# Optimization experiments

Measured on AMD Instinct MI355X. Metric: run time of the kernel, lower is better.

Reference implementation:

```python
import jax, jax.numpy as jnp
import numpy as np

B, T, I, H = 512, 1024, 50, 32  # batch, seq_len, input_size, hidden_size


def setup_inputs() -> dict:
    key = jax.random.key(0)
    ks = jax.random.split(key, 13)
    s = 1.0 / np.sqrt(H)  # PyTorch LSTM/Linear uniform init bound

    def u(k, shape):
        return jax.random.uniform(k, shape, jnp.float32, -s, s)

    return {
        "x": jax.random.normal(ks[0], (B, T, I), jnp.float32),
        # forward direction LSTM params (gate order: i, f, g, o)
        "w_ih_f": u(ks[1], (4 * H, I)),
        "w_hh_f": u(ks[2], (4 * H, H)),
        "b_ih_f": u(ks[3], (4 * H,)),
        "b_hh_f": u(ks[4], (4 * H,)),
        # reverse direction LSTM params
        "w_ih_r": u(ks[5], (4 * H, I)),
        "w_hh_r": u(ks[6], (4 * H, H)),
        "b_ih_r": u(ks[7], (4 * H,)),
        "b_hh_r": u(ks[8], (4 * H,)),
        # FC head
        "fc1_w": u(ks[9], (2 * H, 2 * H)),
        "fc1_b": u(ks[10], (2 * H,)),
        "fc3_w": u(ks[11], (1, 2 * H)),
        "fc3_b": u(ks[12], (1,)),
    }


def _lstm_scan(x_proj, w_hh):
    # x_proj: (T, B, 4H) = precomputed input projections + biases
    b = x_proj.shape[1]
    h0 = jnp.zeros((b, H), x_proj.dtype)
    c0 = jnp.zeros((b, H), x_proj.dtype)

    def step(carry, xp):
        h, c = carry
        z = xp + h @ w_hh.T  # (B, 4H)
        i, f, g, o = jnp.split(z, 4, axis=-1)
        c = jax.nn.sigmoid(f) * c + jax.nn.sigmoid(i) * jnp.tanh(g)
        h = jax.nn.sigmoid(o) * jnp.tanh(c)
        return (h, c), h

    _, hs = jax.lax.scan(step, (h0, c0), x_proj)
    return hs  # (T, B, H)


def reference(x, w_ih_f, w_hh_f, b_ih_f, b_hh_f,
              w_ih_r, w_hh_r, b_ih_r, b_hh_r,
              fc1_w, fc1_b, fc3_w, fc3_b):
    xt = jnp.swapaxes(x, 0, 1)  # (T, B, I) time-major for scan
    # batch all input projections up front (big GEMM instead of per-step)
    pf = xt @ w_ih_f.T + (b_ih_f + b_hh_f)          # (T, B, 4H)
    pr = xt[::-1] @ w_ih_r.T + (b_ih_r + b_hh_r)    # reversed time

    hf = _lstm_scan(pf, w_hh_f)           # (T, B, H)
    hr = _lstm_scan(pr, w_hh_r)[::-1]     # flip back to forward time order

    out = jnp.concatenate([hf, hr], axis=-1)  # (T, B, 2H)
    out = jnp.swapaxes(out, 0, 1)             # (B, T, 2H)
    out = out @ fc1_w.T + fc1_b               # fc1
    # dropout(p=0.2) is identity in eval/inference mode
    out = out @ fc3_w.T + fc3_b               # fc3 -> (B, T, 1)
    return out
```

## Files before the change

kernel.cpp:

```cpp
#include <hip/hip_runtime.h>

#define BB 512
#define TT 1024
#define II 50
#define HH 32
#define CH 16
#define NCH (TT / CH)
#define RSLOT 32

typedef float v2f __attribute__((ext_vector_type(2)));
typedef float v4f __attribute__((ext_vector_type(4)));
typedef short v8s __attribute__((ext_vector_type(8)));

__device__ __forceinline__ float fast_rcp(float x) { return __builtin_amdgcn_rcpf(x); }
__device__ __forceinline__ float sigm(float x) { return fast_rcp(1.f + __expf(-x)); }
__device__ __forceinline__ float tanh_(float x) {
    return 1.f - 2.f * fast_rcp(1.f + __expf(2.f * x));
}
__device__ __forceinline__ short bf16rne(float f) {
    unsigned u = __float_as_uint(f);
    u += 0x7FFF + ((u >> 16) & 1);
    return (short)(u >> 16);
}
__device__ __forceinline__ float rlane(float v, int l) {
    return __int_as_float(__builtin_amdgcn_readlane(__float_as_int(v), l));
}

#if __has_builtin(__builtin_amdgcn_permlane32_swap)
typedef unsigned v2u __attribute__((ext_vector_type(2)));
__device__ __forceinline__ float xhalf_sum(float p) {
    v2u r = __builtin_amdgcn_permlane32_swap(__float_as_uint(p),
                                             __float_as_uint(p), false, false);
    return __uint_as_float(r.x) + __uint_as_float(r.y);
}
#else
__device__ __forceinline__ float xhalf_sum(float p) {
    return p + __shfl_xor(p, 32, 64);
}
#endif

__global__ void init_out_kernel(float* __restrict__ out,
                                const float* __restrict__ fc1_b,
                                const float* __restrict__ fc3_w,
                                const float* __restrict__ fc3_b,
                                int n) {
    int idx = blockIdx.x * blockDim.x + threadIdx.x;
    float b = fc3_b[0];
    #pragma unroll
    for (int k = 0; k < 64; ++k) b += fc3_w[k] * fc1_b[k];
    if (idx < n) out[idx] = b;
}

__global__ void __launch_bounds__(384, 1) lstm_pc_kernel(
    const float* __restrict__ x,
    const float* __restrict__ w_ih_f, const float* __restrict__ w_hh_f,
    const float* __restrict__ b_ih_f, const float* __restrict__ b_hh_f,
    const float* __restrict__ w_ih_r, const float* __restrict__ w_hh_r,
    const float* __restrict__ b_ih_r, const float* __restrict__ b_hh_r,
    const float* __restrict__ fc1_w, const float* __restrict__ fc3_w,
    float* __restrict__ out)
{
    __shared__ float ringF[2][RSLOT * 256];
    __shared__ float hbuf[2][2][HH][65];

    const int tid  = threadIdx.x;
    const int lane = tid & 63;
    const int wave = tid >> 6;
    const int is_prod = (wave >= 4);
    const int sb   = is_prod ? (wave - 4) : (wave >> 1);
    const int b    = blockIdx.x * 2 + sb;
    float* outb = out + (size_t)b * TT;
    float* ring = ringF[sb];

    if (is_prod) {
        const float* xb = x + (size_t)b * TT * II;
        const int nl = lane & 15;
        const int q  = lane >> 4;
        const float* wih[2] = {w_ih_f, w_ih_r};

        v8s Bf[2][8][2];
        #pragma unroll
        for (int d = 0; d < 2; ++d)
            #pragma unroll
            for (int nt = 0; nt < 8; ++nt) {
                const int n = nt * 16 + nl;
                #pragma unroll
                for (int kf = 0; kf < 2; ++kf)
                    #pragma unroll
                    for (int j = 0; j < 8; ++j) {
                        const int k = kf * 32 + q * 8 + j;
                        Bf[d][nt][kf][j] = (k < II) ? bf16rne(wih[d][n * II + k])
                                                    : (short)0;
                    }
            }

        auto cidx = [](int g) -> int {
            return (g < 32) ? 2 * g
                 : (g < 64) ? 2 * (g - 32) + 1
                 : (g < 96) ? 64 + 2 * (g - 64)
                            : 64 + 2 * (g - 96) + 1;
        };

        auto produce_chunk = [&](int c) {
            #pragma unroll
            for (int d = 0; d < 2; ++d) {
                const int S = c * CH + nl;
                const int t = d ? (TT - 1 - S) : S;
                const float* xr = xb + (size_t)t * II;
                v8s A0, A1;
                #pragma unroll
                for (int j = 0; j < 8; ++j) A0[j] = bf16rne(xr[q * 8 + j]);
                #pragma unroll
                for (int j = 0; j < 8; ++j) {
                    const int k = 32 + q * 8 + j;
                    A1[j] = (k < II) ? bf16rne(xr[k]) : (short)0;
                }
                #pragma unroll
                for (int nt = 0; nt < 8; ++nt) {
                    v4f acc = {0.f, 0.f, 0.f, 0.f};
                    acc = __builtin_amdgcn_mfma_f32_16x16x32_bf16(A0, Bf[d][nt][0], acc, 0, 0, 0);
                    acc = __builtin_amdgcn_mfma_f32_16x16x32_bf16(A1, Bf[d][nt][1], acc, 0, 0, 0);
                    const int col = d * 128 + cidx(nt * 16 + nl);
                    #pragma unroll
                    for (int r = 0; r < 4; ++r) {
                        const int slot = (c * CH + q * 4 + r) & (RSLOT - 1);
                        ring[slot * 256 + col] = acc[r];
                    }
                }
            }
        };
        auto flush = [&](int m) {
            if (lane < 32) {
                const int d   = lane >> 4;
                const int idx = lane & 15;
                const int ti  = m * CH + idx;
                const int col = ti & 63;
                float d0 = 0.f, d1 = 0.f, d2 = 0.f, d3 = 0.f;
                #pragma unroll
                for (int k = 0; k < HH; k += 4) {
                    d0 += hbuf[sb][d][k    ][col];
                    d1 += hbuf[sb][d][k + 1][col];
                    d2 += hbuf[sb][d][k + 2][col];
                    d3 += hbuf[sb][d][k + 3][col];
                }
                const int t = d ? (TT - 1 - ti) : ti;
                atomicAdd(&outb[t], (d0 + d1) + (d2 + d3));
            }
        };

        produce_chunk(0);
        __syncthreads();
        for (int n = 0; n < NCH; ++n) {
            if (n + 1 < NCH) produce_chunk(n + 1);
            if (n >= 1) flush(n - 1);
            __syncthreads();
        }
        flush(NCH - 1);
    } else {
        const int d  = wave & 1;
        const int k  = lane & 31;
        const int gh = lane >> 5;
        const float* w_hh = d ? w_hh_r : w_hh_f;
        const float* bi   = d ? b_ih_r : b_ih_f;
        const float* bh   = d ? b_hh_r : b_hh_f;

        const int rowA = gh ? (64 + k) : k;
        const int rowB = gh ? (96 + k) : (32 + k);
        v2f wpA[16], wpB[16];
        #pragma unroll
        for (int j = 0; j < 16; ++j) {
            wpA[j].x = w_hh[rowA * HH + 2 * j];
            wpA[j].y = w_hh[rowA * HH + 2 * j + 1];
            wpB[j].x = w_hh[rowB * HH + 2 * j];
            wpB[j].y = w_hh[rowB * HH + 2 * j + 1];
        }
        const float bA = bi[rowA] + bh[rowA];
        const float bB = bi[rowB] + bh[rowB];
        const float mm = gh ? 2.f : 1.f;
        const float aa = gh ? -1.f : 0.f;

        float wc = 0.f;
        {
            const int j = d * HH + k;
            #pragma unroll
            for (int n = 0; n < 64; ++n) wc += fc3_w[n] * fc1_w[n * 64 + j];
        }

        float c = 0.f;
        float h = 0.f;

        __syncthreads();

        for (int n = 0; n < NCH; ++n) {
            const int slot0 = (n & 1) * CH;
            const int col0  = (n & 3) * CH;
            #pragma unroll
            for (int u = 0; u < CH; ++u) {
                const v2f xz = *(const v2f*)&ring[(slot0 + u) * 256 + d * 128
                                                  + gh * 64 + 2 * k];

                float hs[32];
                #pragma unroll
                for (int j = 0; j < 32; ++j) hs[j] = rlane(h, j);

                v2f aA = (v2f){bA, 0.f};
                v2f aB = (v2f){bB, 0.f};
                #pragma unroll
                for (int j = 0; j < 16; ++j) {
                    const v2f hp = {hs[2 * j], hs[2 * j + 1]};
                    aA = __builtin_elementwise_fma(hp, wpA[j], aA);
                    aB = __builtin_elementwise_fma(hp, wpB[j], aB);
                }
                const float zA = xz.x + aA.x + aA.y;
                const float zB = xz.y + aB.x + aB.y;

                const float actA = fmaf(sigm(zA * mm), mm, aa);
                const float actB = sigm(zB);

                const float pA = xhalf_sum(actA) - actA;
                const float pB = xhalf_sum(actB) - actB;

                const float si = gh ? pA   : actA;
                const float tg = gh ? actA : pA;
                const float sf = gh ? pB   : actB;
                const float so = gh ? actB : pB;

                c = fmaf(sf, c, si * tg);
                h = so * tanh_(c);

                hbuf[sb][d][k][col0 + u] = h * wc;
            }
            __syncthreads();
        }
    }
}

extern "C" void kernel_launch(void* const* d_in, const int* in_sizes, int n_in,
                              void* d_out, int out_size, void* d_ws, size_t ws_size,
                              hipStream_t stream) {
    const float* x      = (const float*)d_in[0];
    const float* w_ih_f = (const float*)d_in[1];
    const float* w_hh_f = (const float*)d_in[2];
    const float* b_ih_f = (const float*)d_in[3];
    const float* b_hh_f = (const float*)d_in[4];
    const float* w_ih_r = (const float*)d_in[5];
    const float* w_hh_r = (const float*)d_in[6];
    const float* b_ih_r = (const float*)d_in[7];
    const float* b_hh_r = (const float*)d_in[8];
    const float* fc1_w  = (const float*)d_in[9];
    const float* fc1_b  = (const float*)d_in[10];
    const float* fc3_w  = (const float*)d_in[11];
    const float* fc3_b  = (const float*)d_in[12];
    float* out = (float*)d_out;

    const int n = BB * TT;
    init_out_kernel<<<(n + 255) / 256, 256, 0, stream>>>(out, fc1_b, fc3_w, fc3_b, n);

    lstm_pc_kernel<<<BB / 2, 384, 0, stream>>>(
        x, w_ih_f, w_hh_f, b_ih_f, b_hh_f,
        w_ih_r, w_hh_r, b_ih_r, b_hh_r,
        fc1_w, fc3_w, out);
}
```

Measured before the change: 425.7 us.

## Fuse producer waves into recurrent waves, removing block-wide barriers

Drops the separate producer waves. Each recurrent wave now computes its own input-projection MFMAs into a private ring and flushes its own output sums, so the per-chunk __syncthreads is gone and the block shrinks from 384 to 256 threads. Global x loads for the next chunks are double-buffered in registers and interleaved with the recurrence. The projection and flush work now sit on the serial critical path of each wave instead of overlapping on other waves, and register pressure rises.

```diff
diff --git a/kernel.cpp b/kernel.cpp
--- a/kernel.cpp
+++ b/kernel.cpp
@@ -51,7 +51,7 @@
     if (idx < n) out[idx] = b;
 }
 
-__global__ void __launch_bounds__(384, 1) lstm_pc_kernel(
+__global__ void __launch_bounds__(256, 1) lstm_fused_kernel(
     const float* __restrict__ x,
     const float* __restrict__ w_ih_f, const float* __restrict__ w_hh_f,
     const float* __restrict__ b_ih_f, const float* __restrict__ b_hh_f,
@@ -60,178 +60,180 @@
     const float* __restrict__ fc1_w, const float* __restrict__ fc3_w,
     float* __restrict__ out)
 {
-    __shared__ float ringF[2][RSLOT * 256];
+    __shared__ float ringF[4][RSLOT * 128];
     __shared__ float hbuf[2][2][HH][65];
 
     const int tid  = threadIdx.x;
     const int lane = tid & 63;
     const int wave = tid >> 6;
-    const int is_prod = (wave >= 4);
-    const int sb   = is_prod ? (wave - 4) : (wave >> 1);
+    const int sb   = wave >> 1;
+    const int d    = wave & 1;
     const int b    = blockIdx.x * 2 + sb;
     float* outb = out + (size_t)b * TT;
-    float* ring = ringF[sb];
-
-    if (is_prod) {
-        const float* xb = x + (size_t)b * TT * II;
-        const int nl = lane & 15;
-        const int q  = lane >> 4;
-        const float* wih[2] = {w_ih_f, w_ih_r};
-
-        v8s Bf[2][8][2];
-        #pragma unroll
-        for (int d = 0; d < 2; ++d)
-            #pragma unroll
-            for (int nt = 0; nt < 8; ++nt) {
-                const int n = nt * 16 + nl;
-                #pragma unroll
-                for (int kf = 0; kf < 2; ++kf)
-                    #pragma unroll
-                    for (int j = 0; j < 8; ++j) {
-                        const int k = kf * 32 + q * 8 + j;
-                        Bf[d][nt][kf][j] = (k < II) ? bf16rne(wih[d][n * II + k])
-                                                    : (short)0;
-                    }
-            }
-
-        auto cidx = [](int g) -> int {
-            return (g < 32) ? 2 * g
-                 : (g < 64) ? 2 * (g - 32) + 1
-                 : (g < 96) ? 64 + 2 * (g - 64)
-                            : 64 + 2 * (g - 96) + 1;
-        };
-
-        auto produce_chunk = [&](int c) {
-            #pragma unroll
-            for (int d = 0; d < 2; ++d) {
-                const int S = c * CH + nl;
-                const int t = d ? (TT - 1 - S) : S;
-                const float* xr = xb + (size_t)t * II;
-                v8s A0, A1;
-                #pragma unroll
-                for (int j = 0; j < 8; ++j) A0[j] = bf16rne(xr[q * 8 + j]);
-                #pragma unroll
-                for (int j = 0; j < 8; ++j) {
-                    const int k = 32 + q * 8 + j;
-                    A1[j] = (k < II) ? bf16rne(xr[k]) : (short)0;
-                }
-                #pragma unroll
-                for (int nt = 0; nt < 8; ++nt) {
-                    v4f acc = {0.f, 0.f, 0.f, 0.f};
-                    acc = __builtin_amdgcn_mfma_f32_16x16x32_bf16(A0, Bf[d][nt][0], acc, 0, 0, 0);
-                    acc = __builtin_amdgcn_mfma_f32_16x16x32_bf16(A1, Bf[d][nt][1], acc, 0, 0, 0);
-                    const int col = d * 128 + cidx(nt * 16 + nl);
-                    #pragma unroll
-                    for (int r = 0; r < 4; ++r) {
-                        const int slot = (c * CH + q * 4 + r) & (RSLOT - 1);
-                        ring[slot * 256 + col] = acc[r];
-                    }
-                }
-            }
-        };
-        auto flush = [&](int m) {
-            if (lane < 32) {
-                const int d   = lane >> 4;
-                const int idx = lane & 15;
-                const int ti  = m * CH + idx;
-                const int col = ti & 63;
-                float d0 = 0.f, d1 = 0.f, d2 = 0.f, d3 = 0.f;
-                #pragma unroll
-                for (int k = 0; k < HH; k += 4) {
-                    d0 += hbuf[sb][d][k    ][col];
-                    d1 += hbuf[sb][d][k + 1][col];
-                    d2 += hbuf[sb][d][k + 2][col];
-                    d3 += hbuf[sb][d][k + 3][col];
-                }
-                const int t = d ? (TT - 1 - ti) : ti;
-                atomicAdd(&outb[t], (d0 + d1) + (d2 + d3));
-            }
-        };
-
-        produce_chunk(0);
-        __syncthreads();
-        for (int n = 0; n < NCH; ++n) {
-            if (n + 1 < NCH) produce_chunk(n + 1);
-            if (n >= 1) flush(n - 1);
-            __syncthreads();
-        }
-        flush(NCH - 1);
-    } else {
-        const int d  = wave & 1;
-        const int k  = lane & 31;
-        const int gh = lane >> 5;
-        const float* w_hh = d ? w_hh_r : w_hh_f;
-        const float* bi   = d ? b_ih_r : b_ih_f;
-        const float* bh   = d ? b_hh_r : b_hh_f;
-
-        const int rowA = gh ? (64 + k) : k;
-        const int rowB = gh ? (96 + k) : (32 + k);
-        v2f wpA[16], wpB[16];
-        #pragma unroll
-        for (int j = 0; j < 16; ++j) {
-            wpA[j].x = w_hh[rowA * HH + 2 * j];
-            wpA[j].y = w_hh[rowA * HH + 2 * j + 1];
-            wpB[j].x = w_hh[rowB * HH + 2 * j];
-            wpB[j].y = w_hh[rowB * HH + 2 * j + 1];
-        }
-        const float bA = bi[rowA] + bh[rowA];
-        const float bB = bi[rowB] + bh[rowB];
-        const float mm = gh ? 2.f : 1.f;
-        const float aa = gh ? -1.f : 0.f;
-
-        float wc = 0.f;
-        {
-            const int j = d * HH + k;
-            #pragma unroll
-            for (int n = 0; n < 64; ++n) wc += fc3_w[n] * fc1_w[n * 64 + j];
-        }
-
-        float c = 0.f;
-        float h = 0.f;
-
-        __syncthreads();
-
-        for (int n = 0; n < NCH; ++n) {
-            const int slot0 = (n & 1) * CH;
-            const int col0  = (n & 3) * CH;
-            #pragma unroll
-            for (int u = 0; u < CH; ++u) {
-                const v2f xz = *(const v2f*)&ring[(slot0 + u) * 256 + d * 128
-                                                  + gh * 64 + 2 * k];
-
-                float hs[32];
-                #pragma unroll
-                for (int j = 0; j < 32; ++j) hs[j] = rlane(h, j);
-
-                v2f aA = (v2f){bA, 0.f};
-                v2f aB = (v2f){bB, 0.f};
-                #pragma unroll
-                for (int j = 0; j < 16; ++j) {
-                    const v2f hp = {hs[2 * j], hs[2 * j + 1]};
-                    aA = __builtin_elementwise_fma(hp, wpA[j], aA);
-                    aB = __builtin_elementwise_fma(hp, wpB[j], aB);
-                }
-                const float zA = xz.x + aA.x + aA.y;
-                const float zB = xz.y + aB.x + aB.y;
-
-                const float actA = fmaf(sigm(zA * mm), mm, aa);
-                const float actB = sigm(zB);
-
-                const float pA = xhalf_sum(actA) - actA;
-                const float pB = xhalf_sum(actB) - actB;
-
-                const float si = gh ? pA   : actA;
-                const float tg = gh ? actA : pA;
-                const float sf = gh ? pB   : actB;
-                const float so = gh ? actB : pB;
-
-                c = fmaf(sf, c, si * tg);
-                h = so * tanh_(c);
-
-                hbuf[sb][d][k][col0 + u] = h * wc;
-            }
-            __syncthreads();
-        }
+    float* ring = ringF[wave];
+
+    const float* xb   = x + (size_t)b * TT * II;
+    const float* wih  = d ? w_ih_r : w_ih_f;
+    const float* w_hh = d ? w_hh_r : w_hh_f;
+    const float* bi   = d ? b_ih_r : b_ih_f;
+    const float* bh   = d ? b_hh_r : b_hh_f;
+
+    const int nl = lane & 15;
+    const int q  = lane >> 4;
+
+    v8s Bf[8][2];
+    #pragma unroll
+    for (int nt = 0; nt < 8; ++nt) {
+        const int n = nt * 16 + nl;
+        #pragma unroll
+        for (int kf = 0; kf < 2; ++kf)
+            #pragma unroll
+            for (int j = 0; j < 8; ++j) {
+                const int kk = kf * 32 + q * 8 + j;
+                Bf[nt][kf][j] = (kk < II) ? bf16rne(wih[n * II + kk]) : (short)0;
+            }
+    }
+
+    auto cidx = [](int g) -> int {
+        return (g < 32) ? 2 * g
+             : (g < 64) ? 2 * (g - 32) + 1
+             : (g < 96) ? 64 + 2 * (g - 64)
+                        : 64 + 2 * (g - 96) + 1;
+    };
+
+    const int k  = lane & 31;
+    const int gh = lane >> 5;
+    const int rowA = gh ? (64 + k) : k;
+    const int rowB = gh ? (96 + k) : (32 + k);
+    v2f wpA[16], wpB[16];
+    #pragma unroll
+    for (int j = 0; j < 16; ++j) {
+        wpA[j].x = w_hh[rowA * HH + 2 * j];
+        wpA[j].y = w_hh[rowA * HH + 2 * j + 1];
+        wpB[j].x = w_hh[rowB * HH + 2 * j];
+        wpB[j].y = w_hh[rowB * HH + 2 * j + 1];
+    }
+    const float bA = bi[rowA] + bh[rowA];
+    const float bB = bi[rowB] + bh[rowB];
+    const float mm = gh ? 2.f : 1.f;
+    const float aa = gh ? -1.f : 0.f;
+
+    float wc = 0.f;
+    {
+        const int j = d * HH + k;
+        #pragma unroll
+        for (int n = 0; n < 64; ++n) wc += fc3_w[n] * fc1_w[n * 64 + j];
+    }
+
+    float xsA[16], xsB[16];
+
+    auto issue_loads = [&](int c, float* xs) {
+        const int S = c * CH + nl;
+        const int t = d ? (TT - 1 - S) : S;
+        const float* xr = xb + (size_t)t * II;
+        #pragma unroll
+        for (int j = 0; j < 8; ++j) xs[j] = xr[q * 8 + j];
+        #pragma unroll
+        for (int j = 0; j < 8; ++j) {
+            const int kk = 32 + q * 8 + j;
+            xs[8 + j] = (kk < II) ? xr[kk] : 0.f;
+        }
+    };
+
+    auto mfma_write = [&](int c, const float* xs) {
+        v8s A0, A1;
+        #pragma unroll
+        for (int j = 0; j < 8; ++j) A0[j] = bf16rne(xs[j]);
+        #pragma unroll
+        for (int j = 0; j < 8; ++j) A1[j] = bf16rne(xs[8 + j]);
+        #pragma unroll
+        for (int nt = 0; nt < 8; ++nt) {
+            v4f acc = {0.f, 0.f, 0.f, 0.f};
+            acc = __builtin_amdgcn_mfma_f32_16x16x32_bf16(A0, Bf[nt][0], acc, 0, 0, 0);
+            acc = __builtin_amdgcn_mfma_f32_16x16x32_bf16(A1, Bf[nt][1], acc, 0, 0, 0);
+            const int col = cidx(nt * 16 + nl);
+            #pragma unroll
+            for (int r = 0; r < 4; ++r) {
+                const int slot = (c * CH + q * 4 + r) & (RSLOT - 1);
+                ring[slot * 128 + col] = acc[r];
+            }
+        }
+    };
+
+    float c_st = 0.f;
+    float h    = 0.f;
+
+    auto run_chunk = [&](int n) {
+        const int slot0 = (n & 1) * CH;
+        const int col0  = (n & 3) * CH;
+        #pragma unroll
+        for (int u = 0; u < CH; ++u) {
+            const v2f xz = *(const v2f*)&ring[(slot0 + u) * 128 + gh * 64 + 2 * k];
+
+            float hs[32];
+            #pragma unroll
+            for (int j = 0; j < 32; ++j) hs[j] = rlane(h, j);
+
+            v2f aA = (v2f){bA, 0.f};
+            v2f aB = (v2f){bB, 0.f};
+            #pragma unroll
+            for (int j = 0; j < 16; ++j) {
+                const v2f hp = {hs[2 * j], hs[2 * j + 1]};
+                aA = __builtin_elementwise_fma(hp, wpA[j], aA);
+                aB = __builtin_elementwise_fma(hp, wpB[j], aB);
+            }
+            const float zA = xz.x + aA.x + aA.y;
+            const float zB = xz.y + aB.x + aB.y;
+
+            const float actA = fmaf(sigm(zA * mm), mm, aa);
+            const float actB = sigm(zB);
+
+            const float pA = xhalf_sum(actA) - actA;
+            const float pB = xhalf_sum(actB) - actB;
+
+            const float si = gh ? pA   : actA;
+            const float tg = gh ? actA : pA;
+            const float sf = gh ? pB   : actB;
+            const float so = gh ? actB : pB;
+
+            c_st = fmaf(sf, c_st, si * tg);
+            h = so * tanh_(c_st);
+
+            hbuf[sb][d][k][col0 + u] = h * wc;
+        }
+    };
+
+    auto flush = [&](int m) {
+        if (lane < CH) {
+            const int ti  = m * CH + lane;
+            const int col = ti & 63;
+            float s0 = 0.f, s1 = 0.f, s2 = 0.f, s3 = 0.f;
+            #pragma unroll
+            for (int kk = 0; kk < HH; kk += 4) {
+                s0 += hbuf[sb][d][kk    ][col];
+                s1 += hbuf[sb][d][kk + 1][col];
+                s2 += hbuf[sb][d][kk + 2][col];
+                s3 += hbuf[sb][d][kk + 3][col];
+            }
+            const int t = d ? (TT - 1 - ti) : ti;
+            atomicAdd(&outb[t], (s0 + s1) + (s2 + s3));
+        }
+    };
+
+    issue_loads(0, xsA);
+    mfma_write(0, xsA);
+    issue_loads(1, xsB);
+
+    for (int n = 0; n < NCH; n += 2) {
+        run_chunk(n);
+        mfma_write(n + 1, xsB);
+        if (n + 2 < NCH) issue_loads(n + 2, xsA);
+        flush(n);
+
+        run_chunk(n + 1);
+        if (n + 2 < NCH) mfma_write(n + 2, xsA);
+        if (n + 3 < NCH) issue_loads(n + 3, xsB);
+        flush(n + 1);
     }
 }
 
@@ -256,7 +258,7 @@
     const int n = BB * TT;
     init_out_kernel<<<(n + 255) / 256, 256, 0, stream>>>(out, fc1_b, fc3_w, fc3_b, n);
 
-    lstm_pc_kernel<<<BB / 2, 384, 0, stream>>>(
+    lstm_fused_kernel<<<BB / 2, 256, 0, stream>>>(
         x, w_ih_f, w_hh_f, b_ih_f, b_hh_f,
         w_ih_r, w_hh_r, b_ih_r, b_hh_r,
         fc1_w, fc3_w, out);
```

Measured after the change: 446.9 us. 5.0% more time.
